# Kernel tuning notes

Hardware: AMD Instinct MI355X
Metric: run time of the kernel (lower is better)

## Reference

```python
import jax, jax.numpy as jnp
import numpy as np

C = 768
H = 12
HD = C // H  # 64


def setup_inputs() -> dict:
    key = jax.random.key(0)
    k1, k2, k3, k4, k5, k6 = jax.random.split(key, 6)
    B, T = 8, 1024
    x = jax.random.normal(k1, (B, T, C), dtype=jnp.float32)
    mask = jax.random.randint(k2, (B, T), 0, 2, dtype=jnp.int32)
    # Linear params stored so that y = x @ W + b (W is [in, out])
    W_attn = jax.random.normal(k3, (C, 3 * C), dtype=jnp.float32) * 0.02
    b_attn = jax.random.normal(k4, (3 * C,), dtype=jnp.float32) * 0.02
    W_proj = jax.random.normal(k5, (C, C), dtype=jnp.float32) * 0.02
    b_proj = jax.random.normal(k6, (C,), dtype=jnp.float32) * 0.02
    return {"x": x, "mask": mask, "W_attn": W_attn, "b_attn": b_attn,
            "W_proj": W_proj, "b_proj": b_proj}


def reference(x, mask, W_attn, b_attn, W_proj, b_proj):
    B, T, _ = x.shape
    qkv = x @ W_attn + b_attn                      # [B, T, 3C]
    q, k, v = jnp.split(qkv, 3, axis=2)            # each [B, T, C]
    # [B, T, C] -> [B, H, T, HD]
    q = q.reshape(B, T, H, HD).transpose(0, 2, 1, 3)
    k = k.reshape(B, T, H, HD).transpose(0, 2, 1, 3)
    v = v.reshape(B, T, H, HD).transpose(0, 2, 1, 3)

    scale = 1.0 / np.sqrt(HD).astype(np.float32)
    att = jnp.einsum('bhqd,bhkd->bhqk', q, k) * scale  # [B, H, T, T]

    causal = jnp.tril(jnp.ones((T, T), dtype=bool))    # [T, T]
    att = jnp.where(causal[None, None], att, -jnp.inf)

    # custom mask: per-(batch, query-row) flag; where mask==0 the whole row
    # of scores is overwritten with 0.0001 (AFTER causal fill, as in torch)
    row_masked = (mask == 0)[:, None, :, None]         # [B, 1, T, 1]
    att = jnp.where(row_masked, jnp.float32(1e-4), att)

    att = jax.nn.softmax(att, axis=-1)
    # dropout layers are identity in eval mode
    y = jnp.einsum('bhqk,bhkd->bhqd', att, v)          # [B, H, T, HD]
    y = y.transpose(0, 2, 1, 3).reshape(B, T, C)
    y = y @ W_proj + b_proj
    return y
```

## Files before the change

### kernel.cpp

```cpp
#include <hip/hip_runtime.h>

#define BQ 8
#define TT 1024
#define CC 768
#define NH 12
#define HD 64
#define BH (BQ*NH)
#define MROWS (BQ*TT)
#define NQKV (3*CC)
#define KD CC

typedef unsigned short u16;
typedef __attribute__((ext_vector_type(4))) short short4v;
typedef __attribute__((ext_vector_type(8))) short short8v;
typedef __attribute__((ext_vector_type(4))) float floatx4;
typedef __attribute__((address_space(1))) const unsigned int gu32;
typedef __attribute__((address_space(3))) unsigned int lu32;

__device__ __forceinline__ float bf2f(u16 u) {
  union { unsigned int i; float f; } c; c.i = ((unsigned int)u) << 16; return c.f;
}
__device__ __forceinline__ u16 f2bf(float f) {
  union { float f; unsigned int i; } c; c.f = f;
  unsigned int i = c.i;
  return (u16)((i + 0x7FFFu + ((i >> 16) & 1u)) >> 16);
}
__device__ __forceinline__ float fast_exp2(float x) {
  return __builtin_amdgcn_exp2f(x);
}
__device__ __forceinline__ void async_ld16(const u16* g, u16* l) {
  __builtin_amdgcn_global_load_lds((gu32*)g, (lu32*)l, 16, 0, 0);
}

#define PREP_CONV 6144
#define PREP_WA   1728

__global__ __launch_bounds__(256) void prep_kernel(
    const float* __restrict__ x, u16* __restrict__ xb,
    const float* __restrict__ Wattn, u16* __restrict__ WtA,
    const float* __restrict__ Wproj, u16* __restrict__ WtP)
{
  __shared__ float tile[32][33];
  int bid = blockIdx.x;
  int tid = threadIdx.x;
  if (bid < PREP_CONV) {
    int i = (bid * 256 + tid) * 4;
    floatx4 v = *(const floatx4*)(x + i);
    short4v o;
    o[0] = (short)f2bf(v[0]); o[1] = (short)f2bf(v[1]);
    o[2] = (short)f2bf(v[2]); o[3] = (short)f2bf(v[3]);
    *(short4v*)(xb + i) = o;
    return;
  }
  const float* in; u16* out; int R, Cc, b2;
  if (bid < PREP_CONV + PREP_WA) { in = Wattn; out = WtA; R = KD; Cc = NQKV; b2 = bid - PREP_CONV; }
  else                           { in = Wproj; out = WtP; R = CC; Cc = CC;   b2 = bid - PREP_CONV - PREP_WA; }
  int ct = Cc >> 5;
  int bx = b2 % ct;
  int by = b2 / ct;
  int tx = tid & 31;
  int ty = tid >> 5;
  int c0 = bx << 5, r0 = by << 5;
#pragma unroll
  for (int s = 0; s < 4; ++s)
    tile[ty + s*8][tx] = in[(size_t)(r0 + ty + s*8) * Cc + c0 + tx];
  __syncthreads();
#pragma unroll
  for (int s = 0; s < 4; ++s)
    out[(size_t)(c0 + ty + s*8) * R + r0 + tx] = f2bf(tile[tx][ty + s*8]);
}

__global__ __launch_bounds__(256) void gemm_bt(
    const u16* __restrict__ A, const u16* __restrict__ Bt,
    const float* __restrict__ bias,
    float* __restrict__ out,
    u16* __restrict__ qo, u16* __restrict__ ko, u16* __restrict__ vo,
    int M, int N, int mode)
{
  __shared__ u16 As[64 * 64];
  __shared__ u16 Bs[128 * 64];

  int tid = threadIdx.x;
  int lane = tid & 63;
  int w = tid >> 6;
  int c = lane & 15;
  int q4 = lane >> 4;

  int mtiles = M >> 6;
  int mt = blockIdx.x % mtiles;
  int nt = blockIdx.x / mtiles;
  int m0 = mt << 6, n0 = nt << 7;

  int wr = (w >> 1) << 5;
  int wc = (w & 1) << 6;

  int srow8 = lane >> 3;
  int ug = ((lane & 7) ^ srow8) << 3;
  const u16* ag = A  + (size_t)(m0 + w * 16 + srow8) * KD + ug;
  const u16* bg = Bt + (size_t)(n0 + w * 32 + srow8) * KD + ug;
  u16* asl = &As[(w * 16) * 64];
  u16* bsl = &Bs[(w * 32) * 64];

  floatx4 acc[2][4];
#pragma unroll
  for (int mi = 0; mi < 2; ++mi)
#pragma unroll
    for (int ni = 0; ni < 4; ++ni) acc[mi][ni] = (floatx4){0.f, 0.f, 0.f, 0.f};

  int c7 = c & 7;

#pragma unroll 1
  for (int kt = 0; kt < KD; kt += 64) {
    async_ld16(ag + kt,              asl);
    async_ld16(ag + kt + 8 * KD,     asl + 8 * 64);
    async_ld16(bg + kt,              bsl);
    async_ld16(bg + kt + 8 * KD,     bsl + 8 * 64);
    async_ld16(bg + kt + 16 * KD,    bsl + 16 * 64);
    async_ld16(bg + kt + 24 * KD,    bsl + 24 * 64);
    __syncthreads();

    short8v af[2][2], bf[4][2];
#pragma unroll
    for (int kc = 0; kc < 2; ++kc) {
      int uoff = ((kc * 4 + q4) ^ c7) << 3;
#pragma unroll
      for (int mi = 0; mi < 2; ++mi)
        af[mi][kc] = *(const short8v*)&As[(wr + mi * 16 + c) * 64 + uoff];
#pragma unroll
      for (int ni = 0; ni < 4; ++ni)
        bf[ni][kc] = *(const short8v*)&Bs[(wc + ni * 16 + c) * 64 + uoff];
    }
#pragma unroll
    for (int kc = 0; kc < 2; ++kc)
#pragma unroll
      for (int mi = 0; mi < 2; ++mi)
#pragma unroll
        for (int ni = 0; ni < 4; ++ni)
          acc[mi][ni] = __builtin_amdgcn_mfma_f32_16x16x32_bf16(af[mi][kc], bf[ni][kc], acc[mi][ni], 0, 0, 0);
    __syncthreads();
  }

  if (mode == 0) {
    int which = (n0 + wc) / CC;
    int nbase = (n0 + wc) - which * CC;
    u16* dst0 = (which == 0) ? qo : ((which == 1) ? ko : vo);
#pragma unroll
    for (int ni = 0; ni < 4; ++ni) {
      int nn = nbase + ni * 16 + c;
      int hh = nn >> 6, dd = nn & 63;
      float bv = bias[which * CC + nn];
#pragma unroll
      for (int mi = 0; mi < 2; ++mi) {
#pragma unroll
        for (int r = 0; r < 4; ++r) {
          int mm = m0 + wr + mi * 16 + q4 * 4 + r;
          int bb = mm >> 10, tt = mm & 1023;
          size_t idx = (((size_t)(bb * NH + hh)) * TT + tt) * HD + dd;
          dst0[idx] = f2bf(acc[mi][ni][r] + bv);
        }
      }
    }
  } else {
#pragma unroll
    for (int ni = 0; ni < 4; ++ni) {
      int nn = n0 + wc + ni * 16 + c;
      float bv = bias[nn];
#pragma unroll
      for (int mi = 0; mi < 2; ++mi) {
#pragma unroll
        for (int r = 0; r < 4; ++r) {
          int mm = m0 + wr + mi * 16 + q4 * 4 + r;
          out[(size_t)mm * N + nn] = acc[mi][ni][r] + bv;
        }
      }
    }
  }
}

__global__ __launch_bounds__(256) void transpose_v(
    const u16* __restrict__ vb, u16* __restrict__ vt)
{
  __shared__ u16 tile[64][72];
  int tid = threadIdx.x;
  int tt0 = (blockIdx.x & 15) << 6;
  int bh = blockIdx.x >> 4;
  {
    int trow = tid >> 2;
    int dchunk = (tid & 3) << 4;
    const u16* src = vb + (((size_t)bh * TT + tt0 + trow) * HD) + dchunk;
    *(short8v*)&tile[trow][dchunk]     = *(const short8v*)src;
    *(short8v*)&tile[trow][dchunk + 8] = *(const short8v*)(src + 8);
  }
  __syncthreads();
  {
    int drow = tid >> 2;
    int tchunk = (tid & 3) << 4;
    short8v a, bv;
#pragma unroll
    for (int j = 0; j < 8; ++j) {
      a[j]  = (short)tile[tchunk + j][drow];
      bv[j] = (short)tile[tchunk + 8 + j][drow];
    }
    u16* dst = vt + ((size_t)bh * HD + drow) * TT + tt0 + tchunk;
    *(short8v*)dst       = a;
    *(short8v*)(dst + 8) = bv;
  }
}

__global__ __launch_bounds__(256) void vk_stats(
    const u16* __restrict__ vtb, const u16* __restrict__ kb,
    float* __restrict__ mv, float* __restrict__ kmaxn)
{
  __shared__ float red[256];
  int bh = blockIdx.x;
  int tid = threadIdx.x;
  int d = tid & 63;
  int g4 = tid >> 6;

  {
    const u16* vp = vtb + ((size_t)bh * HD + d) * TT + g4 * 256;
    float s = 0.f;
#pragma unroll 4
    for (int j = 0; j < 256; j += 8) {
      short8v v = *(const short8v*)(vp + j);
#pragma unroll
      for (int i = 0; i < 8; ++i) s += bf2f((u16)v[i]);
    }
    red[tid] = s;
  }
  __syncthreads();
  if (g4 == 0) mv[bh * HD + d] = (red[d] + red[d + 64] + red[d + 128] + red[d + 192]) * (1.0f / 1024.0f);
  __syncthreads();

  float mx = 0.f;
#pragma unroll 1
  for (int t = tid; t < TT; t += 256) {
    const u16* p = kb + ((size_t)bh * TT + t) * HD;
    float ss = 0.f;
#pragma unroll
    for (int j = 0; j < 64; j += 8) {
      short8v v = *(const short8v*)(p + j);
#pragma unroll
      for (int i = 0; i < 8; ++i) {
        float f = bf2f((u16)v[i]);
        ss = fmaf(f, f, ss);
      }
    }
    mx = fmaxf(mx, ss);
  }
  red[tid] = mx;
  __syncthreads();
  for (int s2 = 128; s2 > 0; s2 >>= 1) {
    if (tid < s2) red[tid] = fmaxf(red[tid], red[tid + s2]);
    __syncthreads();
  }
  if (tid == 0) kmaxn[bh] = sqrtf(red[0]);
}

#define LDW 72
#define SCL 0.18033688f

__global__ __launch_bounds__(256) void attn_kernel(
    const u16* __restrict__ qb, const u16* __restrict__ kb,
    const u16* __restrict__ vtb, const int* __restrict__ mask,
    const float* __restrict__ meanv, const float* __restrict__ kmaxn,
    u16* __restrict__ outb)
{
  __shared__ u16 Ks[64 * LDW];
  __shared__ u16 Vs[64 * LDW];
  __shared__ u16 Ps[4][16 * LDW];

  int tid = threadIdx.x;
  int lane = tid & 63;
  int w = tid >> 6;
  int c = lane & 15;
  int q4 = lane >> 4;

  int pair = blockIdx.x & 7;
  int bh = blockIdx.x >> 3;
  int b = bh / NH;
  int h = bh - b * NH;
  float kmax = kmaxn[bh];

  int srow = tid >> 2;
  int schunk = (tid & 3) << 4;
  const u16* kgp = kb + ((size_t)bh * TT + srow) * HD + schunk;
  const u16* vgp = vtb + ((size_t)bh * HD + srow) * TT + schunk;
  u16* ksw = &Ks[srow * LDW + schunk];
  u16* vsw = &Vs[srow * LDW + schunk];
  u16* pw = &Ps[w][0];

  short8v onesv;
#pragma unroll
  for (int j = 0; j < 8; ++j) onesv[j] = (short)0x3F80;

#pragma unroll 1
  for (int phase = 0; phase < 2; ++phase) {
    int qt = phase ? (15 - pair) : pair;
    int rowbase = (qt << 6) + (w << 4);

    short8v qfrag[2];
    {
      const u16* qp = qb + ((size_t)bh * TT + rowbase + c) * HD + q4 * 8;
      qfrag[0] = *(const short8v*)qp;
      qfrag[1] = *(const short8v*)(qp + 32);
    }

    float q2 = 0.f;
#pragma unroll
    for (int kc = 0; kc < 2; ++kc)
#pragma unroll
      for (int j = 0; j < 8; ++j) {
        float qv = bf2f((u16)qfrag[kc][j]);
        q2 = fmaf(qv, qv, q2);
      }
    q2 += __shfl_xor(q2, 16);
    q2 += __shfl_xor(q2, 32);
    float Mc = sqrtf(q2) * kmax * SCL;

    floatx4 o[4];
#pragma unroll
    for (int i = 0; i < 4; ++i) o[i] = (floatx4){0.f, 0.f, 0.f, 0.f};
    floatx4 o5 = (floatx4){0.f, 0.f, 0.f, 0.f};

    short8v kr0, kr1, vr0, vr1;
    kr0 = *(const short8v*)kgp;
    kr1 = *(const short8v*)(kgp + 8);
    vr0 = *(const short8v*)vgp;
    vr1 = *(const short8v*)(vgp + 8);

#pragma unroll 1
    for (int kt = 0; kt <= qt; ++kt) {
      __syncthreads();
      *(short8v*)ksw = kr0; *(short8v*)(ksw + 8) = kr1;
      *(short8v*)vsw = vr0; *(short8v*)(vsw + 8) = vr1;
      __syncthreads();

      if (kt < qt) {
        const u16* kp = kgp + ((size_t)(kt + 1) << 6) * HD;
        const u16* vp = vgp + ((kt + 1) << 6);
        kr0 = *(const short8v*)kp;
        kr1 = *(const short8v*)(kp + 8);
        vr0 = *(const short8v*)vp;
        vr1 = *(const short8v*)(vp + 8);
      }

      floatx4 s[4];
#pragma unroll
      for (int nt = 0; nt < 4; ++nt) s[nt] = (floatx4){0.f, 0.f, 0.f, 0.f};
#pragma unroll
      for (int kc = 0; kc < 2; ++kc) {
#pragma unroll
        for (int nt = 0; nt < 4; ++nt) {
          short8v kf = *(const short8v*)&Ks[(nt * 16 + c) * LDW + kc * 32 + q4 * 8];
          s[nt] = __builtin_amdgcn_mfma_f32_16x16x32_bf16(kf, qfrag[kc], s[nt], 0, 0, 0);
        }
      }

      int qrl = (w << 4) + c;
#pragma unroll
      for (int nt = 0; nt < 4; ++nt) {
        short4v pk;
#pragma unroll
        for (int r = 0; r < 4; ++r) {
          float sv = s[nt][r];
          if (kt == qt && (nt * 16 + (q4 << 2) + r > qrl)) sv = -INFINITY;
          pk[r] = (short)f2bf(fast_exp2(fmaf(sv, SCL, -Mc)));
        }
        *(short4v*)&pw[c * LDW + nt * 16 + (q4 << 2)] = pk;
      }

#pragma unroll
      for (int kc = 0; kc < 2; ++kc) {
        short8v pf = *(const short8v*)&pw[c * LDW + kc * 32 + q4 * 8];
#pragma unroll
        for (int nt = 0; nt < 4; ++nt) {
          short8v vf = *(const short8v*)&Vs[(nt * 16 + c) * LDW + kc * 32 + q4 * 8];
          o[nt] = __builtin_amdgcn_mfma_f32_16x16x32_bf16(pf, vf, o[nt], 0, 0, 0);
        }
        o5 = __builtin_amdgcn_mfma_f32_16x16x32_bf16(pf, onesv, o5, 0, 0, 0);
      }
    }

    int qrow[4]; bool msk[4]; float inv[4];
#pragma unroll
    for (int r = 0; r < 4; ++r) {
      qrow[r] = rowbase + q4 * 4 + r;
      msk[r] = (mask[b * TT + qrow[r]] == 0);
      inv[r] = 1.f / o5[r];
    }
#pragma unroll
    for (int nt = 0; nt < 4; ++nt) {
      int d = nt * 16 + c;
      float mv = meanv[bh * HD + d];
#pragma unroll
      for (int r = 0; r < 4; ++r) {
        float val = msk[r] ? mv : o[nt][r] * inv[r];
        outb[((size_t)(b * TT + qrow[r])) * CC + h * HD + d] = f2bf(val);
      }
    }
  }
}

extern "C" void kernel_launch(void* const* d_in, const int* in_sizes, int n_in,
                              void* d_out, int out_size, void* d_ws, size_t ws_size,
                              hipStream_t stream)
{
  (void)in_sizes; (void)n_in; (void)out_size; (void)ws_size;
  const float* x     = (const float*)d_in[0];
  const int*   mask  = (const int*)d_in[1];
  const float* Wattn = (const float*)d_in[2];
  const float* battn = (const float*)d_in[3];
  const float* Wproj = (const float*)d_in[4];
  const float* bproj = (const float*)d_in[5];
  float* out = (float*)d_out;

  char* ws = (char*)d_ws;
  size_t off = 0;
  auto alloc = [&](size_t bytes) -> void* {
    void* p = ws + off;
    off += (bytes + 255) & ~(size_t)255;
    return p;
  };
  u16* WtA  = (u16*)alloc((size_t)NQKV * KD * 2);
  u16* WtP  = (u16*)alloc((size_t)CC * CC * 2);
  u16* xb   = (u16*)alloc((size_t)MROWS * CC * 2);
  u16* qbuf = (u16*)alloc((size_t)MROWS * CC * 2);
  u16* kbuf = (u16*)alloc((size_t)MROWS * CC * 2);
  u16* vbuf = (u16*)alloc((size_t)MROWS * CC * 2);
  u16* vtb  = (u16*)alloc((size_t)MROWS * CC * 2);
  u16* abuf = (u16*)alloc((size_t)MROWS * CC * 2);
  float* mv = (float*)alloc((size_t)BH * HD * 4);
  float* kmx = (float*)alloc((size_t)BH * 4);

  prep_kernel<<<8448, 256, 0, stream>>>(x, xb, Wattn, WtA, Wproj, WtP);

  gemm_bt<<<(MROWS/64)*(NQKV/128), 256, 0, stream>>>(
      xb, WtA, battn, nullptr, qbuf, kbuf, vbuf, MROWS, NQKV, 0);

  transpose_v<<<BH * (TT/64), 256, 0, stream>>>(vbuf, vtb);
  vk_stats<<<BH, 256, 0, stream>>>(vtb, kbuf, mv, kmx);

  attn_kernel<<<BH * 8, 256, 0, stream>>>(qbuf, kbuf, vtb, mask, mv, kmx, abuf);

  gemm_bt<<<(MROWS/64)*(CC/128), 256, 0, stream>>>(
      abuf, WtP, bproj, out, nullptr, nullptr, nullptr, MROWS, CC, 1);
}
```

Before: 200.9 us.

## Fuse V transpose and K/V statistics into QKV GEMM epilogue; double-buffer attention tiles

The QKV GEMM epilogue now stages its output tile through shared memory so stores are vectorized. For the V slice it writes V directly in transposed layout. The same epilogue computes per-head K row-norm maxima with atomicMax and V column sums with atomicAdd, which removes the separate transpose_v and vk_stats kernels and the extra V buffer. The attention kernel double-buffers its K/V shared tiles, dropping one barrier per iteration. The costs are atomics on global memory, a zero-init block added to prep, non-deterministic float summation for the mean, and a small safety margin on kmax.

```diff
diff --git a/kernel.cpp b/kernel.cpp
--- a/kernel.cpp
+++ b/kernel.cpp
@@ -34,15 +34,23 @@
 
 #define PREP_CONV 6144
 #define PREP_WA   1728
+#define PREP_WP   576
+#define PREP_TOTAL (PREP_CONV + PREP_WA + PREP_WP)
 
 __global__ __launch_bounds__(256) void prep_kernel(
     const float* __restrict__ x, u16* __restrict__ xb,
     const float* __restrict__ Wattn, u16* __restrict__ WtA,
-    const float* __restrict__ Wproj, u16* __restrict__ WtP)
+    const float* __restrict__ Wproj, u16* __restrict__ WtP,
+    float* __restrict__ mvz, unsigned int* __restrict__ kmxz)
 {
   __shared__ float tile[32][33];
   int bid = blockIdx.x;
   int tid = threadIdx.x;
+  if (bid == PREP_TOTAL) {
+    for (int i = tid; i < BH * HD; i += 256) mvz[i] = 0.f;
+    if (tid < BH) kmxz[tid] = 0u;
+    return;
+  }
   if (bid < PREP_CONV) {
     int i = (bid * 256 + tid) * 4;
     floatx4 v = *(const floatx4*)(x + i);
@@ -75,10 +83,12 @@
     const float* __restrict__ bias,
     float* __restrict__ out,
     u16* __restrict__ qo, u16* __restrict__ ko, u16* __restrict__ vo,
+    float* __restrict__ mvp, unsigned int* __restrict__ kmxp,
     int M, int N, int mode)
 {
-  __shared__ u16 As[64 * 64];
-  __shared__ u16 Bs[128 * 64];
+  __shared__ u16 smem[64 * 64 + 128 * 64];
+  u16* Asm = smem;
+  u16* Bsm = smem + 64 * 64;
 
   int tid = threadIdx.x;
   int lane = tid & 63;
@@ -98,8 +108,8 @@
   int ug = ((lane & 7) ^ srow8) << 3;
   const u16* ag = A  + (size_t)(m0 + w * 16 + srow8) * KD + ug;
   const u16* bg = Bt + (size_t)(n0 + w * 32 + srow8) * KD + ug;
-  u16* asl = &As[(w * 16) * 64];
-  u16* bsl = &Bs[(w * 32) * 64];
+  u16* asl = &Asm[(w * 16) * 64];
+  u16* bsl = &Bsm[(w * 32) * 64];
 
   floatx4 acc[2][4];
 #pragma unroll
@@ -125,10 +135,10 @@
       int uoff = ((kc * 4 + q4) ^ c7) << 3;
 #pragma unroll
       for (int mi = 0; mi < 2; ++mi)
-        af[mi][kc] = *(const short8v*)&As[(wr + mi * 16 + c) * 64 + uoff];
+        af[mi][kc] = *(const short8v*)&Asm[(wr + mi * 16 + c) * 64 + uoff];
 #pragma unroll
       for (int ni = 0; ni < 4; ++ni)
-        bf[ni][kc] = *(const short8v*)&Bs[(wc + ni * 16 + c) * 64 + uoff];
+        bf[ni][kc] = *(const short8v*)&Bsm[(wc + ni * 16 + c) * 64 + uoff];
     }
 #pragma unroll
     for (int kc = 0; kc < 2; ++kc)
@@ -141,23 +151,90 @@
   }
 
   if (mode == 0) {
-    int which = (n0 + wc) / CC;
-    int nbase = (n0 + wc) - which * CC;
-    u16* dst0 = (which == 0) ? qo : ((which == 1) ? ko : vo);
+    int which = n0 / CC;
+    int nbase = n0 - which * CC;
+    int bb = m0 >> 10;
+    int t0 = m0 & 1023;
 #pragma unroll
     for (int ni = 0; ni < 4; ++ni) {
-      int nn = nbase + ni * 16 + c;
-      int hh = nn >> 6, dd = nn & 63;
-      float bv = bias[which * CC + nn];
-#pragma unroll
-      for (int mi = 0; mi < 2; ++mi) {
+      float bv = bias[which * CC + nbase + wc + ni * 16 + c];
+#pragma unroll
+      for (int mi = 0; mi < 2; ++mi)
+#pragma unroll
+        for (int r = 0; r < 4; ++r) acc[mi][ni][r] += bv;
+    }
+    int hw = (nbase + wc) >> 6;
+    int bhw = bb * NH + hw;
+
+    if (which == 1) {
+      float rmax = 0.f;
+#pragma unroll
+      for (int mi = 0; mi < 2; ++mi)
 #pragma unroll
         for (int r = 0; r < 4; ++r) {
-          int mm = m0 + wr + mi * 16 + q4 * 4 + r;
-          int bb = mm >> 10, tt = mm & 1023;
-          size_t idx = (((size_t)(bb * NH + hh)) * TT + tt) * HD + dd;
-          dst0[idx] = f2bf(acc[mi][ni][r] + bv);
-        }
+          float ss = 0.f;
+#pragma unroll
+          for (int ni = 0; ni < 4; ++ni) ss = fmaf(acc[mi][ni][r], acc[mi][ni][r], ss);
+          ss += __shfl_xor(ss, 1); ss += __shfl_xor(ss, 2);
+          ss += __shfl_xor(ss, 4); ss += __shfl_xor(ss, 8);
+          rmax = fmaxf(rmax, ss);
+        }
+      rmax = fmaxf(rmax, __shfl_xor(rmax, 16));
+      rmax = fmaxf(rmax, __shfl_xor(rmax, 32));
+      if (lane == 0) atomicMax(&kmxp[bhw], __float_as_uint(rmax));
+    } else if (which == 2) {
+#pragma unroll
+      for (int ni = 0; ni < 4; ++ni) {
+        float s = 0.f;
+#pragma unroll
+        for (int mi = 0; mi < 2; ++mi)
+#pragma unroll
+          for (int r = 0; r < 4; ++r) s += acc[mi][ni][r];
+        s += __shfl_xor(s, 16); s += __shfl_xor(s, 32);
+        if (q4 == 0) atomicAdd(&mvp[bhw * HD + ni * 16 + c], s);
+      }
+    }
+
+    if (which < 2) {
+      u16* Cs = smem;
+#pragma unroll
+      for (int ni = 0; ni < 4; ++ni)
+#pragma unroll
+        for (int mi = 0; mi < 2; ++mi)
+#pragma unroll
+          for (int r = 0; r < 4; ++r)
+            Cs[(wr + mi * 16 + q4 * 4 + r) * 136 + wc + ni * 16 + c] = f2bf(acc[mi][ni][r]);
+      __syncthreads();
+      u16* dst0 = (which == 0) ? qo : ko;
+#pragma unroll
+      for (int j = 0; j < 4; ++j) {
+        int flat = tid + j * 256;
+        int row = flat >> 4, u = flat & 15;
+        short8v val = *(const short8v*)&Cs[row * 136 + u * 8];
+        int nn2 = nbase + u * 8;
+        int h2 = nn2 >> 6, d2 = nn2 & 63;
+        *(short8v*)&dst0[(((size_t)(bb * NH + h2)) * TT + t0 + row) * HD + d2] = val;
+      }
+    } else {
+      u16* Ct = smem;
+#pragma unroll
+      for (int ni = 0; ni < 4; ++ni)
+#pragma unroll
+        for (int mi = 0; mi < 2; ++mi) {
+          short4v pk;
+#pragma unroll
+          for (int r = 0; r < 4; ++r) pk[r] = (short)f2bf(acc[mi][ni][r]);
+          *(short4v*)&Ct[(wc + ni * 16 + c) * 72 + wr + mi * 16 + q4 * 4] = pk;
+        }
+      __syncthreads();
+#pragma unroll
+      for (int j = 0; j < 4; ++j) {
+        int flat = tid + j * 256;
+        int drow = flat >> 3, u = flat & 7;
+        short8v val = *(const short8v*)&Ct[drow * 72 + u * 8];
+        int nn2 = nbase + drow;
+        int h2 = nn2 >> 6, d2 = nn2 & 63;
+        *(short8v*)&vo[(((size_t)(bb * NH + h2)) * HD + d2) * TT + t0 + u * 8] = val;
       }
     }
   } else {
@@ -177,97 +254,17 @@
   }
 }
 
-__global__ __launch_bounds__(256) void transpose_v(
-    const u16* __restrict__ vb, u16* __restrict__ vt)
-{
-  __shared__ u16 tile[64][72];
-  int tid = threadIdx.x;
-  int tt0 = (blockIdx.x & 15) << 6;
-  int bh = blockIdx.x >> 4;
-  {
-    int trow = tid >> 2;
-    int dchunk = (tid & 3) << 4;
-    const u16* src = vb + (((size_t)bh * TT + tt0 + trow) * HD) + dchunk;
-    *(short8v*)&tile[trow][dchunk]     = *(const short8v*)src;
-    *(short8v*)&tile[trow][dchunk + 8] = *(const short8v*)(src + 8);
-  }
-  __syncthreads();
-  {
-    int drow = tid >> 2;
-    int tchunk = (tid & 3) << 4;
-    short8v a, bv;
-#pragma unroll
-    for (int j = 0; j < 8; ++j) {
-      a[j]  = (short)tile[tchunk + j][drow];
-      bv[j] = (short)tile[tchunk + 8 + j][drow];
-    }
-    u16* dst = vt + ((size_t)bh * HD + drow) * TT + tt0 + tchunk;
-    *(short8v*)dst       = a;
-    *(short8v*)(dst + 8) = bv;
-  }
-}
-
-__global__ __launch_bounds__(256) void vk_stats(
-    const u16* __restrict__ vtb, const u16* __restrict__ kb,
-    float* __restrict__ mv, float* __restrict__ kmaxn)
-{
-  __shared__ float red[256];
-  int bh = blockIdx.x;
-  int tid = threadIdx.x;
-  int d = tid & 63;
-  int g4 = tid >> 6;
-
-  {
-    const u16* vp = vtb + ((size_t)bh * HD + d) * TT + g4 * 256;
-    float s = 0.f;
-#pragma unroll 4
-    for (int j = 0; j < 256; j += 8) {
-      short8v v = *(const short8v*)(vp + j);
-#pragma unroll
-      for (int i = 0; i < 8; ++i) s += bf2f((u16)v[i]);
-    }
-    red[tid] = s;
-  }
-  __syncthreads();
-  if (g4 == 0) mv[bh * HD + d] = (red[d] + red[d + 64] + red[d + 128] + red[d + 192]) * (1.0f / 1024.0f);
-  __syncthreads();
-
-  float mx = 0.f;
-#pragma unroll 1
-  for (int t = tid; t < TT; t += 256) {
-    const u16* p = kb + ((size_t)bh * TT + t) * HD;
-    float ss = 0.f;
-#pragma unroll
-    for (int j = 0; j < 64; j += 8) {
-      short8v v = *(const short8v*)(p + j);
-#pragma unroll
-      for (int i = 0; i < 8; ++i) {
-        float f = bf2f((u16)v[i]);
-        ss = fmaf(f, f, ss);
-      }
-    }
-    mx = fmaxf(mx, ss);
-  }
-  red[tid] = mx;
-  __syncthreads();
-  for (int s2 = 128; s2 > 0; s2 >>= 1) {
-    if (tid < s2) red[tid] = fmaxf(red[tid], red[tid + s2]);
-    __syncthreads();
-  }
-  if (tid == 0) kmaxn[bh] = sqrtf(red[0]);
-}
-
 #define LDW 72
 #define SCL 0.18033688f
 
 __global__ __launch_bounds__(256) void attn_kernel(
     const u16* __restrict__ qb, const u16* __restrict__ kb,
     const u16* __restrict__ vtb, const int* __restrict__ mask,
-    const float* __restrict__ meanv, const float* __restrict__ kmaxn,
+    const float* __restrict__ meanv, const unsigned int* __restrict__ kmaxn,
     u16* __restrict__ outb)
 {
-  __shared__ u16 Ks[64 * LDW];
-  __shared__ u16 Vs[64 * LDW];
+  __shared__ u16 Ks[2][64 * LDW];
+  __shared__ u16 Vs[2][64 * LDW];
   __shared__ u16 Ps[4][16 * LDW];
 
   int tid = threadIdx.x;
@@ -280,14 +277,12 @@
   int bh = blockIdx.x >> 3;
   int b = bh / NH;
   int h = bh - b * NH;
-  float kmax = kmaxn[bh];
+  float kmax = sqrtf(__uint_as_float(kmaxn[bh])) * 1.002f;
 
   int srow = tid >> 2;
   int schunk = (tid & 3) << 4;
   const u16* kgp = kb + ((size_t)bh * TT + srow) * HD + schunk;
   const u16* vgp = vtb + ((size_t)bh * HD + srow) * TT + schunk;
-  u16* ksw = &Ks[srow * LDW + schunk];
-  u16* vsw = &Vs[srow * LDW + schunk];
   u16* pw = &Ps[w][0];
 
   short8v onesv;
@@ -323,17 +318,21 @@
     for (int i = 0; i < 4; ++i) o[i] = (floatx4){0.f, 0.f, 0.f, 0.f};
     floatx4 o5 = (floatx4){0.f, 0.f, 0.f, 0.f};
 
-    short8v kr0, kr1, vr0, vr1;
-    kr0 = *(const short8v*)kgp;
-    kr1 = *(const short8v*)(kgp + 8);
-    vr0 = *(const short8v*)vgp;
-    vr1 = *(const short8v*)(vgp + 8);
+    short8v kr0 = *(const short8v*)kgp;
+    short8v kr1 = *(const short8v*)(kgp + 8);
+    short8v vr0 = *(const short8v*)vgp;
+    short8v vr1 = *(const short8v*)(vgp + 8);
+    __syncthreads();
+    {
+      u16* kd = &Ks[0][srow * LDW + schunk];
+      u16* vd = &Vs[0][srow * LDW + schunk];
+      *(short8v*)kd = kr0; *(short8v*)(kd + 8) = kr1;
+      *(short8v*)vd = vr0; *(short8v*)(vd + 8) = vr1;
+    }
 
 #pragma unroll 1
     for (int kt = 0; kt <= qt; ++kt) {
-      __syncthreads();
-      *(short8v*)ksw = kr0; *(short8v*)(ksw + 8) = kr1;
-      *(short8v*)vsw = vr0; *(short8v*)(vsw + 8) = vr1;
+      int cur = kt & 1;
       __syncthreads();
 
       if (kt < qt) {
@@ -352,7 +351,7 @@
       for (int kc = 0; kc < 2; ++kc) {
 #pragma unroll
         for (int nt = 0; nt < 4; ++nt) {
-          short8v kf = *(const short8v*)&Ks[(nt * 16 + c) * LDW + kc * 32 + q4 * 8];
+          short8v kf = *(const short8v*)&Ks[cur][(nt * 16 + c) * LDW + kc * 32 + q4 * 8];
           s[nt] = __builtin_amdgcn_mfma_f32_16x16x32_bf16(kf, qfrag[kc], s[nt], 0, 0, 0);
         }
       }
@@ -370,12 +369,19 @@
         *(short4v*)&pw[c * LDW + nt * 16 + (q4 << 2)] = pk;
       }
 
+      if (kt < qt) {
+        u16* kd = &Ks[cur ^ 1][srow * LDW + schunk];
+        u16* vd = &Vs[cur ^ 1][srow * LDW + schunk];
+        *(short8v*)kd = kr0; *(short8v*)(kd + 8) = kr1;
+        *(short8v*)vd = vr0; *(short8v*)(vd + 8) = vr1;
+      }
+
 #pragma unroll
       for (int kc = 0; kc < 2; ++kc) {
         short8v pf = *(const short8v*)&pw[c * LDW + kc * 32 + q4 * 8];
 #pragma unroll
         for (int nt = 0; nt < 4; ++nt) {
-          short8v vf = *(const short8v*)&Vs[(nt * 16 + c) * LDW + kc * 32 + q4 * 8];
+          short8v vf = *(const short8v*)&Vs[cur][(nt * 16 + c) * LDW + kc * 32 + q4 * 8];
           o[nt] = __builtin_amdgcn_mfma_f32_16x16x32_bf16(pf, vf, o[nt], 0, 0, 0);
         }
         o5 = __builtin_amdgcn_mfma_f32_16x16x32_bf16(pf, onesv, o5, 0, 0, 0);
@@ -392,7 +398,7 @@
 #pragma unroll
     for (int nt = 0; nt < 4; ++nt) {
       int d = nt * 16 + c;
-      float mv = meanv[bh * HD + d];
+      float mv = meanv[bh * HD + d] * 0.0009765625f;
 #pragma unroll
       for (int r = 0; r < 4; ++r) {
         float val = msk[r] ? mv : o[nt][r] * inv[r];
@@ -427,22 +433,18 @@
   u16* xb   = (u16*)alloc((size_t)MROWS * CC * 2);
   u16* qbuf = (u16*)alloc((size_t)MROWS * CC * 2);
   u16* kbuf = (u16*)alloc((size_t)MROWS * CC * 2);
-  u16* vbuf = (u16*)alloc((size_t)MROWS * CC * 2);
   u16* vtb  = (u16*)alloc((size_t)MROWS * CC * 2);
   u16* abuf = (u16*)alloc((size_t)MROWS * CC * 2);
   float* mv = (float*)alloc((size_t)BH * HD * 4);
-  float* kmx = (float*)alloc((size_t)BH * 4);
-
-  prep_kernel<<<8448, 256, 0, stream>>>(x, xb, Wattn, WtA, Wproj, WtP);
+  unsigned int* kmx = (unsigned int*)alloc((size_t)BH * 4);
+
+  prep_kernel<<<PREP_TOTAL + 1, 256, 0, stream>>>(x, xb, Wattn, WtA, Wproj, WtP, mv, kmx);
 
   gemm_bt<<<(MROWS/64)*(NQKV/128), 256, 0, stream>>>(
-      xb, WtA, battn, nullptr, qbuf, kbuf, vbuf, MROWS, NQKV, 0);
-
-  transpose_v<<<BH * (TT/64), 256, 0, stream>>>(vbuf, vtb);
-  vk_stats<<<BH, 256, 0, stream>>>(vtb, kbuf, mv, kmx);
+      xb, WtA, battn, nullptr, qbuf, kbuf, vtb, mv, kmx, MROWS, NQKV, 0);
 
   attn_kernel<<<BH * 8, 256, 0, stream>>>(qbuf, kbuf, vtb, mask, mv, kmx, abuf);
 
   gemm_bt<<<(MROWS/64)*(CC/128), 256, 0, stream>>>(
-      abuf, WtP, bproj, out, nullptr, nullptr, nullptr, MROWS, CC, 1);
-}
+      abuf, WtP, bproj, out, nullptr, nullptr, nullptr, nullptr, nullptr, MROWS, CC, 1);
+}
```

New measurement: 190.8 us. 5.0% less time.
